# Performance work log

Measured on AMD Instinct MI355X. Metric: run time of the kernel, lower is better.

Reference implementation:

```python
import jax, jax.numpy as jnp
import numpy as np

BN_EPS = 1e-5


def setup_inputs() -> dict:
    key = jax.random.key(0)
    ks = jax.random.split(key, 3)
    B, S, C, H, W = 4, 8, 64, 96, 96
    P = 6
    DIM = 768
    x = jax.random.normal(ks[0], (B, S, C, H, W), dtype=jnp.float32)
    conv_w = jax.random.normal(ks[1], (C, C, 3, 3), dtype=jnp.float32) * 0.05
    conv_b = jnp.zeros((C,), dtype=jnp.float32)
    bn_gamma = jnp.ones((C,), dtype=jnp.float32)
    bn_beta = jnp.zeros((C,), dtype=jnp.float32)
    bn_mean = jnp.zeros((C,), dtype=jnp.float32)
    bn_var = jnp.ones((C,), dtype=jnp.float32)
    proj_w = jax.random.normal(ks[2], (DIM, P * P * C), dtype=jnp.float32) * 0.02
    proj_b = jnp.zeros((DIM,), dtype=jnp.float32)
    mask = jnp.ones((P, P), dtype=jnp.float32)
    return {"x": x, "conv_w": conv_w, "conv_b": conv_b,
            "bn_gamma": bn_gamma, "bn_beta": bn_beta,
            "bn_mean": bn_mean, "bn_var": bn_var,
            "proj_w": proj_w, "proj_b": proj_b,
            "mask": mask, "patch_size": P}


def reference(x, conv_w, conv_b, bn_gamma, bn_beta, bn_mean, bn_var,
              proj_w, proj_b, mask, patch_size):
    B, S, C, H, W = x.shape
    p = patch_size
    Cout = conv_w.shape[0]
    # Fuse the per-frame loop: run conv over all B*S frames at once.
    xf = x.reshape(B * S, C, H, W)
    y = jax.lax.conv_general_dilated(
        xf, conv_w, window_strides=(1, 1), padding=[(1, 1), (1, 1)],
        dimension_numbers=("NCHW", "OIHW", "NCHW"))
    y = y + conv_b[None, :, None, None]
    # BatchNorm2d (eval-mode running stats); Dropout2d is identity at eval.
    inv = jax.lax.rsqrt(bn_var + BN_EPS)
    y = (y - bn_mean[None, :, None, None]) * (bn_gamma * inv)[None, :, None, None] \
        + bn_beta[None, :, None, None]
    y = jax.nn.gelu(y, approximate=False)  # torch GELU default = exact erf
    y = y.reshape(B, S, Cout, H, W)
    # Patch extraction, row-major over (l_idx, r_idx) exactly as the loop.
    pr = H // p  # patches per row
    patches = y.reshape(B, S, Cout, pr, p, pr, p).transpose(0, 1, 3, 5, 2, 4, 6)
    patches = patches.reshape(B, S, pr * pr, Cout, p, p) * mask  # [B,S,P,C,p,p]
    # Flatten(start_dim=2 on [B,S,C,p,p]) + Linear + GELU, batched over patches.
    flat = patches.reshape(B, S, pr * pr, Cout * p * p)
    tokens = jax.nn.gelu(
        jnp.einsum("bsnf,df->bsnd", flat, proj_w) + proj_b, approximate=False)
    return tokens, patches
```

## Files before the change

### kernel.cpp

```cpp
#include <hip/hip_runtime.h>
#include <hip/hip_bf16.h>
#include <math.h>


typedef unsigned short u16;
typedef __bf16 bf16x8 __attribute__((ext_vector_type(8)));
typedef float f32x4 __attribute__((ext_vector_type(4)));

#define NFRM 32
#define CH 64
#define HW 96
#define HWP 98
#define KP 2304
#define DIMN 768
#define MTOK 8192
#define TOKN (MTOK * DIMN)
#define NPAT (MTOK * KP)
#define XHWC_ELEMS ((size_t)NFRM * HWP * HWP * CH)
#define BP_OFF XHWC_ELEMS
#define PW_OFF (BP_OFF + 36864)
#define BSTR 328

static __device__ __forceinline__ u16 f2b(float f) {
  unsigned u = __builtin_bit_cast(unsigned, f);
  u += 0x7fffu + ((u >> 16) & 1u);
  return (u16)(u >> 16);
}
static __device__ __forceinline__ float gelu_f(float x) {
  return 0.5f * x * (1.0f + erff(x * 0.7071067811865476f));
}

typedef __attribute__((address_space(3))) unsigned int lds_uint;
typedef __attribute__((address_space(1))) const unsigned int g_uint;
static __device__ __forceinline__ void gload16(const u16* g, u16* s) {
  __builtin_amdgcn_global_load_lds((g_uint*)g, (lds_uint*)s, 16, 0, 0);
}

__global__ __launch_bounds__(256) void k_transpose(const float* __restrict__ x,
                                                   u16* __restrict__ xhwc) {
  __shared__ u16 tile[96 * 66];
  const int f = blockIdx.x / 96, h = blockIdx.x % 96;
  const int t = threadIdx.x;
  const float* xp = x + (size_t)f * CH * HW * HW + (size_t)h * HW;
#pragma unroll
  for (int k = 0; k < 6; ++k) {
    int e = (k * 256 + t) * 4;
    int ci = e / 96, w = e % 96;
    float4 v = *(const float4*)(xp + (size_t)ci * (HW * HW) + w);
    tile[(w + 0) * 66 + ci] = f2b(v.x);
    tile[(w + 1) * 66 + ci] = f2b(v.y);
    tile[(w + 2) * 66 + ci] = f2b(v.z);
    tile[(w + 3) * 66 + ci] = f2b(v.w);
  }
  __syncthreads();
  u16* op = xhwc + ((size_t)(f * HWP + h + 1) * HWP + 1) * CH;
#pragma unroll
  for (int k = 0; k < 12; ++k) {
    int e2 = (k * 256 + t) * 2;
    int w = e2 >> 6, ci = e2 & 63;
    *(unsigned*)(op + e2) = *(const unsigned*)(&tile[w * 66 + ci]);
  }
}

__global__ __launch_bounds__(256) void k_bpack(const float* __restrict__ w,
                                               u16* __restrict__ bp) {
  int e = blockIdx.x * 256 + threadIdx.x;
  int co = e / 576, r = e - co * 576, tap = r >> 6, ci = r & 63;
  bp[e] = f2b(w[(co * 64 + ci) * 9 + tap]);
}

__global__ __launch_bounds__(256) void k_pw(const float* __restrict__ pw,
                                            u16* __restrict__ dst) {
  int e = (blockIdx.x * 256 + threadIdx.x) * 4;
  float4 v = *(const float4*)(pw + e);
  ushort4 o;
  o.x = f2b(v.x); o.y = f2b(v.y); o.z = f2b(v.z); o.w = f2b(v.w);
  *(ushort4*)(dst + e) = o;
}

template <int T0, int NT>
static __device__ __forceinline__ void conv_tapblock(
    const u16* __restrict__ bw, u16* Bs2, const char* asb,
    f32x4 (&acc)[9][2], const int (&pb)[9],
    const int t, const int wn, const int lm, const int quad) {
  for (int e = t; e < 64 * NT * 8; e += 512) {
    const int co = e / (NT * 8), kk = e - co * (NT * 8);
    *(uint4*)&Bs2[co * BSTR + kk * 8] = *(const uint4*)&bw[co * 576 + T0 * 64 + kk * 8];
  }
  __syncthreads();
#pragma unroll
  for (int tp = 0; tp < NT; ++tp) {
    const int tap = T0 + tp;
    const int di = tap / 3, dj = tap - (tap / 3) * 3;
#pragma unroll
    for (int ks = 0; ks < 2; ++ks) {
      const int kq = ks * 4 + quad;
      const bf16x8 b0 = *(const bf16x8*)&Bs2[(wn * 32 + lm) * BSTR + tp * 64 + ks * 32 + quad * 8];
      const bf16x8 b1 = *(const bf16x8*)&Bs2[(wn * 32 + 16 + lm) * BSTR + tp * 64 + ks * 32 + quad * 8];
#pragma unroll
      for (int mf = 0; mf < 9; ++mf) {
        const int p = pb[mf] + di * 98 + dj;
        const bf16x8 a = *(const bf16x8*)(asb + p * 128 + ((kq ^ (p & 7)) << 4));
        acc[mf][0] = __builtin_amdgcn_mfma_f32_16x16x32_bf16(a, b0, acc[mf][0], 0, 0, 0);
        acc[mf][1] = __builtin_amdgcn_mfma_f32_16x16x32_bf16(a, b1, acc[mf][1], 0, 0, 0);
      }
    }
  }
}

__global__ __launch_bounds__(512, 2) void k_conv(
    const u16* __restrict__ xhwc, const u16* __restrict__ bw,
    const float* __restrict__ cb, const float* __restrict__ gma,
    const float* __restrict__ bta, const float* __restrict__ mu,
    const float* __restrict__ var, const float* __restrict__ msk,
    float* __restrict__ pout) {
  __shared__ alignas(16) u16 As2[8 * 98 * 64];
  __shared__ alignas(16) u16 Bs2[64 * BSTR];
  const int f = blockIdx.x >> 4, pr0 = blockIdx.x & 15;
  const int t = threadIdx.x;
  const int wid = t >> 6, l = t & 63, quad = l >> 4, lm = l & 15;
  const int wm = wid >> 1, wn = wid & 1;

  const u16* sbase = xhwc + ((size_t)f * HWP + pr0 * 6) * (HWP * CH);
  for (int c = wid; c < 98; c += 8) {
    const int p = c * 8 + (l >> 3);
    const int g = (l & 7) ^ (p & 7);
    gload16(sbase + p * 64 + g * 8, &As2[c * 512]);
  }

  int pb[9];
#pragma unroll
  for (int mf = 0; mf < 9; ++mf) {
    const int i16 = wm * 9 + mf;
    pb[mf] = (i16 / 6) * 98 + (i16 % 6) * 16 + lm;
  }
  f32x4 acc[9][2];
#pragma unroll
  for (int mf = 0; mf < 9; ++mf) {
    acc[mf][0] = (f32x4){0.f, 0.f, 0.f, 0.f};
    acc[mf][1] = (f32x4){0.f, 0.f, 0.f, 0.f};
  }
  const char* asb = (const char*)As2;

  conv_tapblock<0, 5>(bw, Bs2, asb, acc, pb, t, wn, lm, quad);
  __syncthreads();
  conv_tapblock<5, 4>(bw, Bs2, asb, acc, pb, t, wn, lm, quad);

#pragma unroll
  for (int nf = 0; nf < 2; ++nf) {
    const int co = wn * 32 + nf * 16 + lm;
    const float scv = gma[co] * rsqrtf(var[co] + 1e-5f);
    const float b2v = (cb[co] - mu[co]) * scv + bta[co];
#pragma unroll
    for (int mf = 0; mf < 9; ++mf) {
#pragma unroll
      for (int rg = 0; rg < 4; ++rg) {
        const int ml = wm * 144 + mf * 16 + quad * 4 + rg;
        const int rr = ml / 96, w = ml - rr * 96;
        const int n = pr0 * 16 + w / 6;
        const int jj = rr * 6 + (w - (w / 6) * 6);
        float v = acc[mf][nf][rg] * scv + b2v;
        v = gelu_f(v) * msk[jj];
        pout[((size_t)(f * 256 + n) * 64 + co) * 36 + jj] = v;
      }
    }
  }
}

__global__ __launch_bounds__(256) void k_cvt(const float* __restrict__ pat,
                                             u16* __restrict__ abf) {
  int e = (blockIdx.x * 256 + threadIdx.x) * 4;
  float4 v = *(const float4*)(pat + e);
  ushort4 o;
  o.x = f2b(v.x); o.y = f2b(v.y); o.z = f2b(v.z); o.w = f2b(v.w);
  *(ushort4*)(abf + e) = o;
}

__global__ __launch_bounds__(256) void k_gemm(const u16* __restrict__ A,
                                              const u16* __restrict__ Bt,
                                              const float* __restrict__ pb,
                                              float* __restrict__ out) {
  __shared__ alignas(16) u16 As[128 * 32];
  __shared__ alignas(16) u16 Bs[64 * 32];
  const int bn = blockIdx.x % 12, bm = blockIdx.x / 12;
  const int m0 = bm * 128, n0 = bn * 64;
  const int t = threadIdx.x, wv = t >> 6, l = t & 63, quad = l >> 4, lm = l & 15;

  const int crow = l >> 2, cg = (l & 3) * 8;
  const u16* aS0 = A + (size_t)(m0 + wv * 32 + crow) * KP + cg;
  const u16* aS1 = A + (size_t)(m0 + wv * 32 + 16 + crow) * KP + cg;
  const u16* bS = Bt + (size_t)(n0 + wv * 16 + crow) * KP + cg;
  u16* aD0 = &As[wv * 1024];
  u16* aD1 = &As[wv * 1024 + 512];
  u16* bD = &Bs[wv * 512];

  f32x4 acc[2][4];
#pragma unroll
  for (int s = 0; s < 2; ++s)
#pragma unroll
    for (int u = 0; u < 4; ++u) acc[s][u] = (f32x4){0.f, 0.f, 0.f, 0.f};

  for (int k0 = 0; k0 < KP; k0 += 32) {
    __syncthreads();
    gload16(aS0 + k0, aD0);
    gload16(aS1 + k0, aD1);
    gload16(bS + k0, bD);
    __syncthreads();
    const int ko = quad * 8;
    const bf16x8 a0 = *(const bf16x8*)&As[(wv * 32 + lm) * 32 + ko];
    const bf16x8 a1 = *(const bf16x8*)&As[(wv * 32 + 16 + lm) * 32 + ko];
#pragma unroll
    for (int u = 0; u < 4; ++u) {
      const bf16x8 b = *(const bf16x8*)&Bs[(u * 16 + lm) * 32 + ko];
      acc[0][u] = __builtin_amdgcn_mfma_f32_16x16x32_bf16(a0, b, acc[0][u], 0, 0, 0);
      acc[1][u] = __builtin_amdgcn_mfma_f32_16x16x32_bf16(a1, b, acc[1][u], 0, 0, 0);
    }
  }
#pragma unroll
  for (int u = 0; u < 4; ++u) {
    const int n = n0 + u * 16 + lm;
    const float bias = pb[n];
#pragma unroll
    for (int s = 0; s < 2; ++s) {
#pragma unroll
      for (int rg = 0; rg < 4; ++rg) {
        const int m = m0 + wv * 32 + s * 16 + quad * 4 + rg;
        out[(size_t)m * DIMN + n] = gelu_f(acc[s][u][rg] + bias);
      }
    }
  }
}

extern "C" void kernel_launch(void* const* d_in, const int* in_sizes, int n_in,
                              void* d_out, int out_size, void* d_ws, size_t ws_size,
                              hipStream_t stream) {
  const float* x = (const float*)d_in[0];
  const float* conv_w = (const float*)d_in[1];
  const float* conv_b = (const float*)d_in[2];
  const float* bn_gamma = (const float*)d_in[3];
  const float* bn_beta = (const float*)d_in[4];
  const float* bn_mean = (const float*)d_in[5];
  const float* bn_var = (const float*)d_in[6];
  const float* proj_w = (const float*)d_in[7];
  const float* proj_b = (const float*)d_in[8];
  const float* mask = (const float*)d_in[9];
  float* out = (float*)d_out;
  float* patches = out + TOKN;
  u16* ws = (u16*)d_ws;
  u16* xhwc = ws;
  u16* bp = ws + BP_OFF;
  u16* pw = ws + PW_OFF;

  hipMemsetAsync(d_ws, 0, XHWC_ELEMS * sizeof(u16), stream);
  k_transpose<<<NFRM * HW, 256, 0, stream>>>(x, xhwc);
  k_bpack<<<144, 256, 0, stream>>>(conv_w, bp);
  k_pw<<<1728, 256, 0, stream>>>(proj_w, pw);
  k_conv<<<NFRM * 16, 512, 0, stream>>>(xhwc, bp, conv_b, bn_gamma, bn_beta,
                                        bn_mean, bn_var, mask, patches);
  k_cvt<<<18432, 256, 0, stream>>>(patches, xhwc);
  k_gemm<<<64 * 12, 256, 0, stream>>>(xhwc, pw, proj_b, out);
}
```

Before: 356.6 us.

## Split conv tiles in half-rows with LDS-staged coalesced output; widen GEMM K-step

The conv kernel now processes half a patch row per 256-thread block (twice as many blocks), loads weights in three row-of-taps phases, and stages the GELU output in LDS so patches are written with contiguous float4 stores instead of scattered scalar stores. The GEMM kernel doubles its K step to 64 with XOR-swizzled LDS tiles, halving the number of barrier pairs per K loop. The aim is better store coalescing, more parallelism and fewer syncs, at the cost of larger LDS use per block and extra halo loads.

Measured after the change: 320.4 us. 1.11x faster.

```diff
diff --git a/kernel.cpp b/kernel.cpp
--- a/kernel.cpp
+++ b/kernel.cpp
@@ -19,7 +19,7 @@
 #define XHWC_ELEMS ((size_t)NFRM * HWP * HWP * CH)
 #define BP_OFF XHWC_ELEMS
 #define PW_OFF (BP_OFF + 36864)
-#define BSTR 328
+#define BSTR 200
 
 static __device__ __forceinline__ u16 f2b(float f) {
   unsigned u = __builtin_bit_cast(unsigned, f);
@@ -78,61 +78,36 @@
   *(ushort4*)(dst + e) = o;
 }
 
-template <int T0, int NT>
-static __device__ __forceinline__ void conv_tapblock(
-    const u16* __restrict__ bw, u16* Bs2, const char* asb,
-    f32x4 (&acc)[9][2], const int (&pb)[9],
-    const int t, const int wn, const int lm, const int quad) {
-  for (int e = t; e < 64 * NT * 8; e += 512) {
-    const int co = e / (NT * 8), kk = e - co * (NT * 8);
-    *(uint4*)&Bs2[co * BSTR + kk * 8] = *(const uint4*)&bw[co * 576 + T0 * 64 + kk * 8];
-  }
-  __syncthreads();
-#pragma unroll
-  for (int tp = 0; tp < NT; ++tp) {
-    const int tap = T0 + tp;
-    const int di = tap / 3, dj = tap - (tap / 3) * 3;
-#pragma unroll
-    for (int ks = 0; ks < 2; ++ks) {
-      const int kq = ks * 4 + quad;
-      const bf16x8 b0 = *(const bf16x8*)&Bs2[(wn * 32 + lm) * BSTR + tp * 64 + ks * 32 + quad * 8];
-      const bf16x8 b1 = *(const bf16x8*)&Bs2[(wn * 32 + 16 + lm) * BSTR + tp * 64 + ks * 32 + quad * 8];
-#pragma unroll
-      for (int mf = 0; mf < 9; ++mf) {
-        const int p = pb[mf] + di * 98 + dj;
-        const bf16x8 a = *(const bf16x8*)(asb + p * 128 + ((kq ^ (p & 7)) << 4));
-        acc[mf][0] = __builtin_amdgcn_mfma_f32_16x16x32_bf16(a, b0, acc[mf][0], 0, 0, 0);
-        acc[mf][1] = __builtin_amdgcn_mfma_f32_16x16x32_bf16(a, b1, acc[mf][1], 0, 0, 0);
-      }
-    }
-  }
-}
-
-__global__ __launch_bounds__(512, 2) void k_conv(
+__global__ __launch_bounds__(256, 2) void k_conv(
     const u16* __restrict__ xhwc, const u16* __restrict__ bw,
     const float* __restrict__ cb, const float* __restrict__ gma,
     const float* __restrict__ bta, const float* __restrict__ mu,
     const float* __restrict__ var, const float* __restrict__ msk,
     float* __restrict__ pout) {
-  __shared__ alignas(16) u16 As2[8 * 98 * 64];
-  __shared__ alignas(16) u16 Bs2[64 * BSTR];
-  const int f = blockIdx.x >> 4, pr0 = blockIdx.x & 15;
-  const int t = threadIdx.x;
-  const int wid = t >> 6, l = t & 63, quad = l >> 4, lm = l & 15;
-  const int wm = wid >> 1, wn = wid & 1;
-
-  const u16* sbase = xhwc + ((size_t)f * HWP + pr0 * 6) * (HWP * CH);
-  for (int c = wid; c < 98; c += 8) {
-    const int p = c * 8 + (l >> 3);
-    const int g = (l & 7) ^ (p & 7);
-    gload16(sbase + p * 64 + g * 8, &As2[c * 512]);
+  __shared__ alignas(16) char SMEM[76800];
+  u16* Asm = (u16*)SMEM;
+  u16* Bsm = (u16*)(SMEM + 51200);
+  float* Fsm = (float*)SMEM;
+
+  const int bx = blockIdx.x;
+  const int f = bx >> 5, rem = bx & 31, pr = rem >> 1, half = rem & 1;
+  const int t = threadIdx.x, wv = t >> 6, l = t & 63, quad = l >> 4, lm = l & 15;
+  const int wm = wv >> 1, wn = wv & 1;
+
+  const u16* sbase = xhwc + (((size_t)f * HWP + pr * 6) * HWP + half * 48) * CH;
+  const int pc = l >> 3;
+  const int gsw = (l & 7) ^ pc;
+  for (int c = wv; c < 50; c += 4) {
+    const int p = c * 8 + pc;
+    const int row = p / 50, ac = p - row * 50;
+    gload16(sbase + ((size_t)row * HWP + ac) * CH + gsw * 8, Asm + c * 512);
   }
 
   int pb[9];
 #pragma unroll
   for (int mf = 0; mf < 9; ++mf) {
     const int i16 = wm * 9 + mf;
-    pb[mf] = (i16 / 6) * 98 + (i16 % 6) * 16 + lm;
+    pb[mf] = (i16 / 3) * 50 + (i16 % 3) * 16 + lm;
   }
   f32x4 acc[9][2];
 #pragma unroll
@@ -140,12 +115,36 @@
     acc[mf][0] = (f32x4){0.f, 0.f, 0.f, 0.f};
     acc[mf][1] = (f32x4){0.f, 0.f, 0.f, 0.f};
   }
-  const char* asb = (const char*)As2;
-
-  conv_tapblock<0, 5>(bw, Bs2, asb, acc, pb, t, wn, lm, quad);
+
+#pragma unroll
+  for (int ph = 0; ph < 3; ++ph) {
+    if (ph > 0) __syncthreads();
+    for (int e = t; e < 1536; e += 256) {
+      const int co = e / 24, kk = e - co * 24;
+      *(uint4*)&Bsm[co * BSTR + kk * 8] =
+          *(const uint4*)&bw[co * 576 + ph * 192 + kk * 8];
+    }
+    __syncthreads();
+#pragma unroll
+    for (int tp = 0; tp < 3; ++tp) {
+      const int di = ph, dj = tp;
+#pragma unroll
+      for (int ks = 0; ks < 2; ++ks) {
+        const int kq = ks * 4 + quad;
+        const bf16x8 b0 = *(const bf16x8*)&Bsm[(wn * 32 + lm) * BSTR + tp * 64 + ks * 32 + quad * 8];
+        const bf16x8 b1 = *(const bf16x8*)&Bsm[(wn * 32 + 16 + lm) * BSTR + tp * 64 + ks * 32 + quad * 8];
+#pragma unroll
+        for (int mf = 0; mf < 9; ++mf) {
+          const int p = pb[mf] + di * 50 + dj;
+          const bf16x8 a = *(const bf16x8*)&Asm[p * 64 + ((kq ^ (p & 7)) << 3)];
+          acc[mf][0] = __builtin_amdgcn_mfma_f32_16x16x32_bf16(a, b0, acc[mf][0], 0, 0, 0);
+          acc[mf][1] = __builtin_amdgcn_mfma_f32_16x16x32_bf16(a, b1, acc[mf][1], 0, 0, 0);
+        }
+      }
+    }
+  }
+
   __syncthreads();
-  conv_tapblock<5, 4>(bw, Bs2, asb, acc, pb, t, wn, lm, quad);
-
 #pragma unroll
   for (int nf = 0; nf < 2; ++nf) {
     const int co = wn * 32 + nf * 16 + lm;
@@ -155,15 +154,22 @@
     for (int mf = 0; mf < 9; ++mf) {
 #pragma unroll
       for (int rg = 0; rg < 4; ++rg) {
-        const int ml = wm * 144 + mf * 16 + quad * 4 + rg;
-        const int rr = ml / 96, w = ml - rr * 96;
-        const int n = pr0 * 16 + w / 6;
-        const int jj = rr * 6 + (w - (w / 6) * 6);
+        const int sp = wm * 144 + mf * 16 + quad * 4 + rg;
+        const int orow = sp / 48, oc = sp - orow * 48;
+        const int nl = oc / 6, pj = oc - nl * 6;
+        const int jj = orow * 6 + pj;
         float v = acc[mf][nf][rg] * scv + b2v;
         v = gelu_f(v) * msk[jj];
-        pout[((size_t)(f * 256 + n) * 64 + co) * 36 + jj] = v;
-      }
-    }
+        Fsm[nl * 2304 + co * 36 + jj] = v;
+      }
+    }
+  }
+  __syncthreads();
+  float* pbase = pout + (size_t)(f * 256 + pr * 16 + half * 8) * KP;
+#pragma unroll
+  for (int k = 0; k < 18; ++k) {
+    const int li = t + k * 256;
+    *(float4*)&pbase[li * 4] = *(const float4*)&Fsm[li * 4];
   }
 }
 
@@ -180,19 +186,13 @@
                                               const u16* __restrict__ Bt,
                                               const float* __restrict__ pb,
                                               float* __restrict__ out) {
-  __shared__ alignas(16) u16 As[128 * 32];
-  __shared__ alignas(16) u16 Bs[64 * 32];
+  __shared__ alignas(16) u16 As[128 * 64];
+  __shared__ alignas(16) u16 Bs[64 * 64];
   const int bn = blockIdx.x % 12, bm = blockIdx.x / 12;
   const int m0 = bm * 128, n0 = bn * 64;
   const int t = threadIdx.x, wv = t >> 6, l = t & 63, quad = l >> 4, lm = l & 15;
-
-  const int crow = l >> 2, cg = (l & 3) * 8;
-  const u16* aS0 = A + (size_t)(m0 + wv * 32 + crow) * KP + cg;
-  const u16* aS1 = A + (size_t)(m0 + wv * 32 + 16 + crow) * KP + cg;
-  const u16* bS = Bt + (size_t)(n0 + wv * 16 + crow) * KP + cg;
-  u16* aD0 = &As[wv * 1024];
-  u16* aD1 = &As[wv * 1024 + 512];
-  u16* bD = &Bs[wv * 512];
+  const int pc = l >> 3;
+  const int gsw = (l & 7) ^ pc;
 
   f32x4 acc[2][4];
 #pragma unroll
@@ -200,20 +200,29 @@
 #pragma unroll
     for (int u = 0; u < 4; ++u) acc[s][u] = (f32x4){0.f, 0.f, 0.f, 0.f};
 
-  for (int k0 = 0; k0 < KP; k0 += 32) {
+  for (int k0 = 0; k0 < KP; k0 += 64) {
     __syncthreads();
-    gload16(aS0 + k0, aD0);
-    gload16(aS1 + k0, aD1);
-    gload16(bS + k0, bD);
+    for (int c = wv; c < 24; c += 4) {
+      if (c < 16) {
+        const int row = c * 8 + pc;
+        gload16(A + (size_t)(m0 + row) * KP + k0 + gsw * 8, As + c * 512);
+      } else {
+        const int row = (c - 16) * 8 + pc;
+        gload16(Bt + (size_t)(n0 + row) * KP + k0 + gsw * 8, Bs + (c - 16) * 512);
+      }
+    }
     __syncthreads();
-    const int ko = quad * 8;
-    const bf16x8 a0 = *(const bf16x8*)&As[(wv * 32 + lm) * 32 + ko];
-    const bf16x8 a1 = *(const bf16x8*)&As[(wv * 32 + 16 + lm) * 32 + ko];
-#pragma unroll
-    for (int u = 0; u < 4; ++u) {
-      const bf16x8 b = *(const bf16x8*)&Bs[(u * 16 + lm) * 32 + ko];
-      acc[0][u] = __builtin_amdgcn_mfma_f32_16x16x32_bf16(a0, b, acc[0][u], 0, 0, 0);
-      acc[1][u] = __builtin_amdgcn_mfma_f32_16x16x32_bf16(a1, b, acc[1][u], 0, 0, 0);
+#pragma unroll
+    for (int ks = 0; ks < 2; ++ks) {
+      const int gx = ((ks * 4 + quad) ^ (lm & 7)) << 3;
+      const bf16x8 a0 = *(const bf16x8*)&As[(wv * 32 + lm) * 64 + gx];
+      const bf16x8 a1 = *(const bf16x8*)&As[(wv * 32 + 16 + lm) * 64 + gx];
+#pragma unroll
+      for (int u = 0; u < 4; ++u) {
+        const bf16x8 b = *(const bf16x8*)&Bs[(u * 16 + lm) * 64 + gx];
+        acc[0][u] = __builtin_amdgcn_mfma_f32_16x16x32_bf16(a0, b, acc[0][u], 0, 0, 0);
+        acc[1][u] = __builtin_amdgcn_mfma_f32_16x16x32_bf16(a1, b, acc[1][u], 0, 0, 0);
+      }
     }
   }
 #pragma unroll
@@ -255,7 +264,7 @@
   k_transpose<<<NFRM * HW, 256, 0, stream>>>(x, xhwc);
   k_bpack<<<144, 256, 0, stream>>>(conv_w, bp);
   k_pw<<<1728, 256, 0, stream>>>(proj_w, pw);
-  k_conv<<<NFRM * 16, 512, 0, stream>>>(xhwc, bp, conv_b, bn_gamma, bn_beta,
+  k_conv<<<NFRM * 32, 256, 0, stream>>>(xhwc, bp, conv_b, bn_gamma, bn_beta,
                                         bn_mean, bn_var, mask, patches);
   k_cvt<<<18432, 256, 0, stream>>>(patches, xhwc);
   k_gemm<<<64 * 12, 256, 0, stream>>>(xhwc, pw, proj_b, out);
```
